# Kernel tuning notes

Measured on AMD Instinct MI355X. Metric: run time of the kernel, lower is better.

Reference implementation:

```python
import jax, jax.numpy as jnp
import numpy as np

SL, BS, E, H, PF, STRIDE, SHIFT = 2048, 2, 1024, 16, 16, 1, 0
DH = E // H  # 64


def setup_inputs() -> dict:
    key = jax.random.key(0)
    ks = jax.random.split(key, 6)
    s = 0.02
    return {
        'x': jax.random.normal(ks[0], (SL, BS, E), jnp.float32),
        'ln_g': jnp.ones((E,), jnp.float32),
        'ln_b': jnp.zeros((E,), jnp.float32),
        'Wq': jax.random.normal(ks[1], (E, E), jnp.float32) * s,
        'bq': jnp.zeros((E,), jnp.float32),
        'Wk': jax.random.normal(ks[2], (E, E), jnp.float32) * s,
        'bk': jnp.zeros((E,), jnp.float32),
        'Wv': jax.random.normal(ks[3], (E, E), jnp.float32) * s,
        'bv': jnp.zeros((E,), jnp.float32),
        'Wo': jax.random.normal(ks[4], (E, E), jnp.float32) * s,
        'bo': jnp.zeros((E,), jnp.float32),
    }


def _layernorm(x, g, b, eps=1e-5):
    m = x.mean(-1, keepdims=True)
    v = jnp.var(x, axis=-1, keepdims=True)
    return (x - m) * jax.lax.rsqrt(v + eps) * g + b


def _sparsify(context, h):
    # faithful to sparsify(): r = (arange(h)+1)*stride - pf + shift (+ arange(pf)), mod c
    c = context.shape[0]
    base = (jnp.arange(h) + 1) * STRIDE - PF + SHIFT          # [h]
    idx = (base[None, :] + jnp.arange(PF)[:, None]) % c       # [pf, h]
    return context[idx.reshape(-1)].reshape(PF, h, context.shape[1], context.shape[2])


def reference(x, ln_g, ln_b, Wq, bq, Wk, bk, Wv, bv, Wo, bo):
    sl, bs, e = x.shape
    residual = x
    xn = _layernorm(x, ln_g, ln_b)
    # gather pf-sized local context window per query position (modular wrap)
    fetch = _sparsify(xn, sl)                                  # [pf, sl, bs, E]
    # per-token query (length-1) attending to its pf gathered keys
    q = (xn @ Wq + bq).reshape(sl, bs, H, DH)                  # [sl,bs,H,dh]
    k = (fetch @ Wk + bk).reshape(PF, sl, bs, H, DH)           # [pf,sl,bs,H,dh]
    v = (fetch @ Wv + bv).reshape(PF, sl, bs, H, DH)
    scale = 1.0 / jnp.sqrt(jnp.float32(DH))
    scores = jnp.einsum('sbhd,psbhd->sbhp', q, k) * scale      # [sl,bs,H,pf]
    attn = jax.nn.softmax(scores, axis=-1)
    out = jnp.einsum('sbhp,psbhd->sbhd', attn, v).reshape(sl, bs, e)
    out = out @ Wo + bo                                        # output projection
    # dropout is a no-op in eval
    return residual + out
```

## Files before the change

### kernel.cpp

```cpp
#include <hip/hip_runtime.h>
#include <cstdint>
#include <cstddef>

#define SLEN 2048
#define BSZ  2
#define EDIM 1024
#define NHEAD 16
#define DHEAD 64
#define PFW  16
#define NTOK (SLEN*BSZ)

#define BM 128
#define BN 128
#define BK 32

typedef __attribute__((ext_vector_type(8))) short short8;
typedef __attribute__((ext_vector_type(4))) float floatx4;

__device__ __forceinline__ short f2bf(float f) {
  union { float f; uint32_t u; } v; v.f = f;
  uint32_t r = v.u + 0x7fffu + ((v.u >> 16) & 1u);
  return (short)(r >> 16);
}
__device__ __forceinline__ float bf2f(short s) {
  union { uint32_t u; float f; } v; v.u = ((uint32_t)(uint16_t)s) << 16;
  return v.f;
}

__device__ __forceinline__ void async16(const void* g, void* l) {
  __builtin_amdgcn_global_load_lds((const __attribute__((address_space(1))) void*)g,
                                   (__attribute__((address_space(3))) void*)l,
                                   16, 0, 0);
}

__global__ __launch_bounds__(256) void transpose_kernel(
    const float* __restrict__ W0, const float* __restrict__ W1,
    const float* __restrict__ W2, const float* __restrict__ W3,
    short* __restrict__ Wt_base)
{
  const int z = blockIdx.z;
  const float* W = (z == 0) ? W0 : (z == 1) ? W1 : (z == 2) ? W2 : W3;
  short* Wt = Wt_base + (size_t)z * EDIM * EDIM;

  __shared__ float tile[32][33];
  const int tx = threadIdx.x & 31;
  const int ty = threadIdx.x >> 5;
  const int n0 = blockIdx.x * 32;
  const int k0 = blockIdx.y * 32;

#pragma unroll
  for (int i = 0; i < 4; ++i)
    tile[ty + i * 8][tx] = W[(size_t)(k0 + ty + i * 8) * EDIM + n0 + tx];
  __syncthreads();
#pragma unroll
  for (int i = 0; i < 4; ++i)
    Wt[(size_t)(n0 + ty + i * 8) * EDIM + k0 + tx] = f2bf(tile[tx][ty + i * 8]);
}

__global__ __launch_bounds__(256) void layernorm_kernel(
    const float* __restrict__ x, const float* __restrict__ g,
    const float* __restrict__ b, short* __restrict__ xn)
{
  const int row = blockIdx.x;
  const int tid = threadIdx.x;
  const float4 v = ((const float4*)(x + (size_t)row * EDIM))[tid];

  float s  = v.x + v.y + v.z + v.w;
  float ss = v.x * v.x + v.y * v.y + v.z * v.z + v.w * v.w;
#pragma unroll
  for (int off = 32; off; off >>= 1) {
    s  += __shfl_xor(s, off);
    ss += __shfl_xor(ss, off);
  }
  __shared__ float ws_s[4], ws_ss[4];
  const int lane = tid & 63, wave = tid >> 6;
  if (lane == 0) { ws_s[wave] = s; ws_ss[wave] = ss; }
  __syncthreads();
  s  = ws_s[0] + ws_s[1] + ws_s[2] + ws_s[3];
  ss = ws_ss[0] + ws_ss[1] + ws_ss[2] + ws_ss[3];

  const float mean = s * (1.0f / EDIM);
  const float var  = ss * (1.0f / EDIM) - mean * mean;
  const float rs   = rsqrtf(var + 1e-5f);

  const float4 gv = ((const float4*)g)[tid];
  const float4 bv = ((const float4*)b)[tid];
  short4 o;
  o.x = f2bf((v.x - mean) * rs * gv.x + bv.x);
  o.y = f2bf((v.y - mean) * rs * gv.y + bv.y);
  o.z = f2bf((v.z - mean) * rs * gv.z + bv.z);
  o.w = f2bf((v.w - mean) * rs * gv.w + bv.w);
  ((short4*)(xn + (size_t)row * EDIM))[tid] = o;
}

__device__ __forceinline__ void gemm_mainloop(
    const short* __restrict__ A, const short* __restrict__ Bt, int K,
    int bm, int bn, short* As, short* Bs, floatx4 (&acc)[4][4])
{
  const int tid  = threadIdx.x;
  const int lane = tid & 63;
  const int wave = tid >> 6;

  const int lrow = lane >> 2;
  const int lcol = (lane & 3) * 8;
  const short* gA0 = A  + (size_t)(bm + wave * 32 + lrow) * K + lcol;
  const short* gA1 = gA0 + (size_t)16 * K;
  const short* gB0 = Bt + (size_t)(bn + wave * 32 + lrow) * K + lcol;
  const short* gB1 = gB0 + (size_t)16 * K;
  short* lA0 = As + wave * 1024;
  short* lA1 = lA0 + 512;
  short* lB0 = Bs + wave * 1024;
  short* lB1 = lB0 + 512;

  const int wm = (wave >> 1) * 64;
  const int wn = (wave & 1) * 64;
  const int fr = lane & 15;
  const int fq = (lane >> 4) * 8;

  for (int k0 = 0; k0 < K; k0 += BK) {
    async16(gA0, lA0); async16(gA1, lA1);
    async16(gB0, lB0); async16(gB1, lB1);
    gA0 += BK; gA1 += BK; gB0 += BK; gB1 += BK;
    __syncthreads();

    short8 af[4], bf[4];
#pragma unroll
    for (int mi = 0; mi < 4; ++mi)
      af[mi] = *(const short8*)(As + (size_t)(wm + mi * 16 + fr) * BK + fq);
#pragma unroll
    for (int ni = 0; ni < 4; ++ni)
      bf[ni] = *(const short8*)(Bs + (size_t)(wn + ni * 16 + fr) * BK + fq);
#pragma unroll
    for (int mi = 0; mi < 4; ++mi)
#pragma unroll
      for (int ni = 0; ni < 4; ++ni)
        acc[mi][ni] = __builtin_amdgcn_mfma_f32_16x16x32_bf16(
            af[mi], bf[ni], acc[mi][ni], 0, 0, 0);
    __syncthreads();
  }
}

__global__ __launch_bounds__(256) void gemm_qkv(
    const short* __restrict__ xn, const short* __restrict__ Wt_base,
    const float* __restrict__ bq, const float* __restrict__ bk,
    const float* __restrict__ bv, short* __restrict__ qkv_base)
{
  __shared__ short As[BM * BK];
  __shared__ short Bs[BN * BK];
  const int z = blockIdx.z;
  const short* Bt   = Wt_base + (size_t)z * EDIM * EDIM;
  const float* bias = (z == 0) ? bq : (z == 1) ? bk : bv;
  short* out        = qkv_base + (size_t)z * NTOK * EDIM;

  const int bm = blockIdx.x * BM;
  const int bn = blockIdx.y * BN;
  floatx4 acc[4][4];
#pragma unroll
  for (int i = 0; i < 4; ++i)
#pragma unroll
    for (int j = 0; j < 4; ++j) { floatx4 zz = {0.f, 0.f, 0.f, 0.f}; acc[i][j] = zz; }

  gemm_mainloop(xn, Bt, EDIM, bm, bn, As, Bs, acc);

  const int lane = threadIdx.x & 63;
  const int wave = threadIdx.x >> 6;
  const int wm = (wave >> 1) * 64, wn = (wave & 1) * 64;
  const int r0 = bm + wm + ((lane >> 4) * 4);
  const int c0 = bn + wn + (lane & 15);
#pragma unroll
  for (int mi = 0; mi < 4; ++mi)
#pragma unroll
    for (int ni = 0; ni < 4; ++ni) {
      const floatx4 v = acc[mi][ni];
      const int col = c0 + ni * 16;
      const float bb = bias[col];
#pragma unroll
      for (int r = 0; r < 4; ++r) {
        const int row = r0 + mi * 16 + r;
        out[(size_t)row * EDIM + col] = f2bf(v[r] + bb);
      }
    }
}

__global__ __launch_bounds__(256) void gemm_o(
    const short* __restrict__ Aattn, const short* __restrict__ Wot,
    const float* __restrict__ bo, const float* __restrict__ residual,
    float* __restrict__ out)
{
  __shared__ short As[BM * BK];
  __shared__ short Bs[BN * BK];
  const int bm = blockIdx.x * BM;
  const int bn = blockIdx.y * BN;
  floatx4 acc[4][4];
#pragma unroll
  for (int i = 0; i < 4; ++i)
#pragma unroll
    for (int j = 0; j < 4; ++j) { floatx4 zz = {0.f, 0.f, 0.f, 0.f}; acc[i][j] = zz; }

  gemm_mainloop(Aattn, Wot, EDIM, bm, bn, As, Bs, acc);

  const int lane = threadIdx.x & 63;
  const int wave = threadIdx.x >> 6;
  const int wm = (wave >> 1) * 64, wn = (wave & 1) * 64;
  const int r0 = bm + wm + ((lane >> 4) * 4);
  const int c0 = bn + wn + (lane & 15);
#pragma unroll
  for (int mi = 0; mi < 4; ++mi)
#pragma unroll
    for (int ni = 0; ni < 4; ++ni) {
      const floatx4 v = acc[mi][ni];
      const int col = c0 + ni * 16;
      const float bb = bo[col];
#pragma unroll
      for (int r = 0; r < 4; ++r) {
        const int row = r0 + mi * 16 + r;
        const size_t idx = (size_t)row * EDIM + col;
        out[idx] = residual[idx] + v[r] + bb;
      }
    }
}

#define VT_LD 80
#define PB_LD 40

__global__ __launch_bounds__(256) void attn_mfma(
    const short* __restrict__ Q, const short* __restrict__ K,
    const short* __restrict__ V, short* __restrict__ O)
{
  const int tid  = threadIdx.x;
  const int lane = tid & 63;
  const int wave = tid >> 6;
  const int quad = lane >> 4;
  const int l16  = lane & 15;

  const int bh = blockIdx.y;
  const int h  = bh & (NHEAD - 1);
  const int b  = bh >> 4;
  const int s_blk = blockIdx.x * 64;
  const int col0  = h * DHEAD;

  __shared__ __align__(16) short VT[64 * VT_LD];
  __shared__ __align__(16) short Pb[4][16 * PB_LD];

  for (int task = tid; task < 320; task += 256) {
    const int kp  = task >> 3;
    const int dg  = task & 7;
    const int kk0 = kp * 2;
    int sA = s_blk - 15 + kk0;
    int sB = sA + 1;
    if (sA < 0) sA += SLEN;  if (sA >= SLEN) sA -= SLEN;
    if (sB < 0) sB += SLEN;  if (sB >= SLEN) sB -= SLEN;
    const short8 vA = *(const short8*)(V + (size_t)(sA * BSZ + b) * EDIM + col0 + dg * 8);
    const short8 vB = *(const short8*)(V + (size_t)(sB * BSZ + b) * EDIM + col0 + dg * 8);
#pragma unroll
    for (int j = 0; j < 8; ++j) {
      const int d = dg * 8 + j;
      const uint32_t pack = (uint32_t)(uint16_t)vA[j] | ((uint32_t)(uint16_t)vB[j] << 16);
      *(uint32_t*)&VT[d * VT_LD + kk0] = pack;
    }
  }

  const int sw = s_blk + wave * 16;
  short8 aq[2];
  {
    const size_t base = (size_t)((sw + l16) * BSZ + b) * EDIM + col0 + quad * 8;
    aq[0] = *(const short8*)(Q + base);
    aq[1] = *(const short8*)(Q + base + 32);
  }
  short8 bkf[2][2];
#pragma unroll
  for (int T = 0; T < 2; ++T) {
    int ks = sw - 15 + T * 16 + l16;
    if (ks < 0) ks += SLEN;
    if (ks >= SLEN) ks -= SLEN;
    const size_t base = (size_t)(ks * BSZ + b) * EDIM + col0 + quad * 8;
    bkf[T][0] = *(const short8*)(K + base);
    bkf[T][1] = *(const short8*)(K + base + 32);
  }

  floatx4 S[2];
  { floatx4 zz = {0.f, 0.f, 0.f, 0.f}; S[0] = zz; S[1] = zz; }
#pragma unroll
  for (int T = 0; T < 2; ++T) {
    S[T] = __builtin_amdgcn_mfma_f32_16x16x32_bf16(aq[0], bkf[T][0], S[T], 0, 0, 0);
    S[T] = __builtin_amdgcn_mfma_f32_16x16x32_bf16(aq[1], bkf[T][1], S[T], 0, 0, 0);
  }

  float sc[2][4];
#pragma unroll
  for (int T = 0; T < 2; ++T)
#pragma unroll
    for (int r = 0; r < 4; ++r) {
      const int m = quad * 4 + r;
      const int c = T * 16 + l16;
      const int d = c - m;
      sc[T][r] = (d >= 0 && d <= 15) ? S[T][r] * 0.125f : -1e30f;
    }
  float mx[4], sm[4];
#pragma unroll
  for (int r = 0; r < 4; ++r) mx[r] = fmaxf(sc[0][r], sc[1][r]);
#pragma unroll
  for (int off = 1; off <= 8; off <<= 1)
#pragma unroll
    for (int r = 0; r < 4; ++r) mx[r] = fmaxf(mx[r], __shfl_xor(mx[r], off));
  float p[2][4];
#pragma unroll
  for (int r = 0; r < 4; ++r) {
    p[0][r] = __expf(sc[0][r] - mx[r]);
    p[1][r] = __expf(sc[1][r] - mx[r]);
    sm[r] = p[0][r] + p[1][r];
  }
#pragma unroll
  for (int off = 1; off <= 8; off <<= 1)
#pragma unroll
    for (int r = 0; r < 4; ++r) sm[r] += __shfl_xor(sm[r], off);

  __syncthreads();

  short* Pw = Pb[wave];
#pragma unroll
  for (int T = 0; T < 2; ++T)
#pragma unroll
    for (int r = 0; r < 4; ++r) {
      const int m = quad * 4 + r;
      const int c = T * 16 + l16;
      Pw[m * PB_LD + c] = f2bf(p[T][r]);
    }
  __syncthreads();
  const short8 ap = *(const short8*)(Pw + l16 * PB_LD + quad * 8);

  floatx4 Oacc[4];
  { floatx4 zz = {0.f, 0.f, 0.f, 0.f}; Oacc[0] = zz; Oacc[1] = zz; Oacc[2] = zz; Oacc[3] = zz; }
#pragma unroll
  for (int nt = 0; nt < 4; ++nt) {
    const short8 bv = *(const short8*)(VT + (nt * 16 + l16) * VT_LD + wave * 16 + quad * 8);
    Oacc[nt] = __builtin_amdgcn_mfma_f32_16x16x32_bf16(ap, bv, Oacc[nt], 0, 0, 0);
  }

#pragma unroll
  for (int nt = 0; nt < 4; ++nt)
#pragma unroll
    for (int r = 0; r < 4; ++r) {
      const int m = quad * 4 + r;
      const size_t idx = (size_t)((sw + m) * BSZ + b) * EDIM + col0 + nt * 16 + l16;
      O[idx] = f2bf(Oacc[nt][r] / sm[r]);
    }
}

extern "C" void kernel_launch(void* const* d_in, const int* in_sizes, int n_in,
                              void* d_out, int out_size, void* d_ws, size_t ws_size,
                              hipStream_t stream) {
  const float* x    = (const float*)d_in[0];
  const float* ln_g = (const float*)d_in[1];
  const float* ln_b = (const float*)d_in[2];
  const float* Wq   = (const float*)d_in[3];
  const float* bq   = (const float*)d_in[4];
  const float* Wk   = (const float*)d_in[5];
  const float* bk   = (const float*)d_in[6];
  const float* Wv   = (const float*)d_in[7];
  const float* bv   = (const float*)d_in[8];
  const float* Wo   = (const float*)d_in[9];
  const float* bo   = (const float*)d_in[10];
  float* out = (float*)d_out;

  char* ws = (char*)d_ws;
  short* xn   = (short*)(ws);
  short* Wt   = (short*)(ws + ((size_t)8  << 20));
  short* QKV  = (short*)(ws + ((size_t)16 << 20));
  short* attn = (short*)(ws + ((size_t)40 << 20));

  transpose_kernel<<<dim3(32, 32, 4), 256, 0, stream>>>(Wq, Wk, Wv, Wo, Wt);
  layernorm_kernel<<<NTOK, 256, 0, stream>>>(x, ln_g, ln_b, xn);
  gemm_qkv<<<dim3(NTOK / BM, EDIM / BN, 3), 256, 0, stream>>>(xn, Wt, bq, bk, bv, QKV);
  attn_mfma<<<dim3(SLEN / 64, BSZ * NHEAD), 256, 0, stream>>>(
      QKV, QKV + (size_t)NTOK * EDIM, QKV + (size_t)2 * NTOK * EDIM, attn);
  gemm_o<<<dim3(NTOK / BM, EDIM / BN), 256, 0, stream>>>(
      attn, Wt + (size_t)3 * EDIM * EDIM, bo, x, out);
}
```

Measured before the change: 162.1 us.

## Merge layernorm and weight transpose into one launch; shrink output GEMM tile to 64 rows

The layernorm and the four weight-transpose launches are merged into one prep kernel whose block index picks which job each block does, removing one kernel launch and letting both jobs share the GPU. The output projection GEMM tile drops from 128x128 to 64x128, doubling its grid from 256 to 512 blocks so more of the CUs are busy. The shared mainloop helper is inlined into each GEMM. The smaller tile lowers data reuse per block and adds more global loads in exchange for the extra parallelism.

```diff
diff --git a/kernel.cpp b/kernel.cpp
--- a/kernel.cpp
+++ b/kernel.cpp
@@ -10,8 +10,6 @@
 #define PFW  16
 #define NTOK (SLEN*BSZ)
 
-#define BM 128
-#define BN 128
 #define BK 32
 
 typedef __attribute__((ext_vector_type(8))) short short8;
@@ -33,110 +31,64 @@
                                    16, 0, 0);
 }
 
-__global__ __launch_bounds__(256) void transpose_kernel(
+__global__ __launch_bounds__(256) void prep_kernel(
+    const float* __restrict__ x, const float* __restrict__ g,
+    const float* __restrict__ b, short* __restrict__ xn,
     const float* __restrict__ W0, const float* __restrict__ W1,
     const float* __restrict__ W2, const float* __restrict__ W3,
     short* __restrict__ Wt_base)
 {
-  const int z = blockIdx.z;
-  const float* W = (z == 0) ? W0 : (z == 1) ? W1 : (z == 2) ? W2 : W3;
-  short* Wt = Wt_base + (size_t)z * EDIM * EDIM;
-
-  __shared__ float tile[32][33];
-  const int tx = threadIdx.x & 31;
-  const int ty = threadIdx.x >> 5;
-  const int n0 = blockIdx.x * 32;
-  const int k0 = blockIdx.y * 32;
-
-#pragma unroll
-  for (int i = 0; i < 4; ++i)
-    tile[ty + i * 8][tx] = W[(size_t)(k0 + ty + i * 8) * EDIM + n0 + tx];
-  __syncthreads();
-#pragma unroll
-  for (int i = 0; i < 4; ++i)
-    Wt[(size_t)(n0 + ty + i * 8) * EDIM + k0 + tx] = f2bf(tile[tx][ty + i * 8]);
-}
-
-__global__ __launch_bounds__(256) void layernorm_kernel(
-    const float* __restrict__ x, const float* __restrict__ g,
-    const float* __restrict__ b, short* __restrict__ xn)
-{
-  const int row = blockIdx.x;
+  const int bid = blockIdx.x;
   const int tid = threadIdx.x;
-  const float4 v = ((const float4*)(x + (size_t)row * EDIM))[tid];
-
-  float s  = v.x + v.y + v.z + v.w;
-  float ss = v.x * v.x + v.y * v.y + v.z * v.z + v.w * v.w;
-#pragma unroll
-  for (int off = 32; off; off >>= 1) {
-    s  += __shfl_xor(s, off);
-    ss += __shfl_xor(ss, off);
-  }
-  __shared__ float ws_s[4], ws_ss[4];
-  const int lane = tid & 63, wave = tid >> 6;
-  if (lane == 0) { ws_s[wave] = s; ws_ss[wave] = ss; }
-  __syncthreads();
-  s  = ws_s[0] + ws_s[1] + ws_s[2] + ws_s[3];
-  ss = ws_ss[0] + ws_ss[1] + ws_ss[2] + ws_ss[3];
-
-  const float mean = s * (1.0f / EDIM);
-  const float var  = ss * (1.0f / EDIM) - mean * mean;
-  const float rs   = rsqrtf(var + 1e-5f);
-
-  const float4 gv = ((const float4*)g)[tid];
-  const float4 bv = ((const float4*)b)[tid];
-  short4 o;
-  o.x = f2bf((v.x - mean) * rs * gv.x + bv.x);
-  o.y = f2bf((v.y - mean) * rs * gv.y + bv.y);
-  o.z = f2bf((v.z - mean) * rs * gv.z + bv.z);
-  o.w = f2bf((v.w - mean) * rs * gv.w + bv.w);
-  ((short4*)(xn + (size_t)row * EDIM))[tid] = o;
-}
-
-__device__ __forceinline__ void gemm_mainloop(
-    const short* __restrict__ A, const short* __restrict__ Bt, int K,
-    int bm, int bn, short* As, short* Bs, floatx4 (&acc)[4][4])
-{
-  const int tid  = threadIdx.x;
-  const int lane = tid & 63;
-  const int wave = tid >> 6;
-
-  const int lrow = lane >> 2;
-  const int lcol = (lane & 3) * 8;
-  const short* gA0 = A  + (size_t)(bm + wave * 32 + lrow) * K + lcol;
-  const short* gA1 = gA0 + (size_t)16 * K;
-  const short* gB0 = Bt + (size_t)(bn + wave * 32 + lrow) * K + lcol;
-  const short* gB1 = gB0 + (size_t)16 * K;
-  short* lA0 = As + wave * 1024;
-  short* lA1 = lA0 + 512;
-  short* lB0 = Bs + wave * 1024;
-  short* lB1 = lB0 + 512;
-
-  const int wm = (wave >> 1) * 64;
-  const int wn = (wave & 1) * 64;
-  const int fr = lane & 15;
-  const int fq = (lane >> 4) * 8;
-
-  for (int k0 = 0; k0 < K; k0 += BK) {
-    async16(gA0, lA0); async16(gA1, lA1);
-    async16(gB0, lB0); async16(gB1, lB1);
-    gA0 += BK; gA1 += BK; gB0 += BK; gB1 += BK;
-    __syncthreads();
-
-    short8 af[4], bf[4];
-#pragma unroll
-    for (int mi = 0; mi < 4; ++mi)
-      af[mi] = *(const short8*)(As + (size_t)(wm + mi * 16 + fr) * BK + fq);
-#pragma unroll
-    for (int ni = 0; ni < 4; ++ni)
-      bf[ni] = *(const short8*)(Bs + (size_t)(wn + ni * 16 + fr) * BK + fq);
-#pragma unroll
-    for (int mi = 0; mi < 4; ++mi)
-#pragma unroll
-      for (int ni = 0; ni < 4; ++ni)
-        acc[mi][ni] = __builtin_amdgcn_mfma_f32_16x16x32_bf16(
-            af[mi], bf[ni], acc[mi][ni], 0, 0, 0);
-    __syncthreads();
+
+  if (bid < NTOK) {
+    const int row = bid;
+    const float4 v = ((const float4*)(x + (size_t)row * EDIM))[tid];
+    float s  = v.x + v.y + v.z + v.w;
+    float ss = v.x * v.x + v.y * v.y + v.z * v.z + v.w * v.w;
+#pragma unroll
+    for (int off = 32; off; off >>= 1) {
+      s  += __shfl_xor(s, off);
+      ss += __shfl_xor(ss, off);
+    }
+    __shared__ float ws_s[4], ws_ss[4];
+    const int lane = tid & 63, wave = tid >> 6;
+    if (lane == 0) { ws_s[wave] = s; ws_ss[wave] = ss; }
+    __syncthreads();
+    s  = ws_s[0] + ws_s[1] + ws_s[2] + ws_s[3];
+    ss = ws_ss[0] + ws_ss[1] + ws_ss[2] + ws_ss[3];
+
+    const float mean = s * (1.0f / EDIM);
+    const float var  = ss * (1.0f / EDIM) - mean * mean;
+    const float rs   = rsqrtf(var + 1e-5f);
+
+    const float4 gv = ((const float4*)g)[tid];
+    const float4 bv = ((const float4*)b)[tid];
+    short4 o;
+    o.x = f2bf((v.x - mean) * rs * gv.x + bv.x);
+    o.y = f2bf((v.y - mean) * rs * gv.y + bv.y);
+    o.z = f2bf((v.z - mean) * rs * gv.z + bv.z);
+    o.w = f2bf((v.w - mean) * rs * gv.w + bv.w);
+    ((short4*)(xn + (size_t)row * EDIM))[tid] = o;
+  } else {
+    const int t = bid - NTOK;
+    const int z = t >> 10;
+    const int rem = t & 1023;
+    const int n0 = (rem & 31) * 32;
+    const int k0 = (rem >> 5) * 32;
+    const float* W = (z == 0) ? W0 : (z == 1) ? W1 : (z == 2) ? W2 : W3;
+    short* Wt = Wt_base + (size_t)z * EDIM * EDIM;
+
+    __shared__ float tile[32][33];
+    const int tx = tid & 31;
+    const int ty = tid >> 5;
+#pragma unroll
+    for (int i = 0; i < 4; ++i)
+      tile[ty + i * 8][tx] = W[(size_t)(k0 + ty + i * 8) * EDIM + n0 + tx];
+    __syncthreads();
+#pragma unroll
+    for (int i = 0; i < 4; ++i)
+      Wt[(size_t)(n0 + ty + i * 8) * EDIM + k0 + tx] = f2bf(tile[tx][ty + i * 8]);
   }
 }
 
@@ -145,26 +97,63 @@
     const float* __restrict__ bq, const float* __restrict__ bk,
     const float* __restrict__ bv, short* __restrict__ qkv_base)
 {
-  __shared__ short As[BM * BK];
-  __shared__ short Bs[BN * BK];
+  __shared__ short As[128 * BK];
+  __shared__ short Bs[128 * BK];
   const int z = blockIdx.z;
   const short* Bt   = Wt_base + (size_t)z * EDIM * EDIM;
   const float* bias = (z == 0) ? bq : (z == 1) ? bk : bv;
   short* out        = qkv_base + (size_t)z * NTOK * EDIM;
 
-  const int bm = blockIdx.x * BM;
-  const int bn = blockIdx.y * BN;
+  const int bm = blockIdx.x * 128;
+  const int bn = blockIdx.y * 128;
+  const int tid  = threadIdx.x;
+  const int lane = tid & 63;
+  const int wave = tid >> 6;
+
   floatx4 acc[4][4];
 #pragma unroll
   for (int i = 0; i < 4; ++i)
 #pragma unroll
     for (int j = 0; j < 4; ++j) { floatx4 zz = {0.f, 0.f, 0.f, 0.f}; acc[i][j] = zz; }
 
-  gemm_mainloop(xn, Bt, EDIM, bm, bn, As, Bs, acc);
-
-  const int lane = threadIdx.x & 63;
-  const int wave = threadIdx.x >> 6;
-  const int wm = (wave >> 1) * 64, wn = (wave & 1) * 64;
+  const int lrow = lane >> 2;
+  const int lcol = (lane & 3) * 8;
+  const short* gA0 = xn + (size_t)(bm + wave * 32 + lrow) * EDIM + lcol;
+  const short* gA1 = gA0 + (size_t)16 * EDIM;
+  const short* gB0 = Bt + (size_t)(bn + wave * 32 + lrow) * EDIM + lcol;
+  const short* gB1 = gB0 + (size_t)16 * EDIM;
+  short* lA0 = As + wave * 1024;
+  short* lA1 = lA0 + 512;
+  short* lB0 = Bs + wave * 1024;
+  short* lB1 = lB0 + 512;
+
+  const int wm = (wave >> 1) * 64;
+  const int wn = (wave & 1) * 64;
+  const int fr = lane & 15;
+  const int fq = (lane >> 4) * 8;
+
+  for (int k0 = 0; k0 < EDIM; k0 += BK) {
+    async16(gA0, lA0); async16(gA1, lA1);
+    async16(gB0, lB0); async16(gB1, lB1);
+    gA0 += BK; gA1 += BK; gB0 += BK; gB1 += BK;
+    __syncthreads();
+
+    short8 af[4], bf[4];
+#pragma unroll
+    for (int mi = 0; mi < 4; ++mi)
+      af[mi] = *(const short8*)(As + (size_t)(wm + mi * 16 + fr) * BK + fq);
+#pragma unroll
+    for (int ni = 0; ni < 4; ++ni)
+      bf[ni] = *(const short8*)(Bs + (size_t)(wn + ni * 16 + fr) * BK + fq);
+#pragma unroll
+    for (int mi = 0; mi < 4; ++mi)
+#pragma unroll
+      for (int ni = 0; ni < 4; ++ni)
+        acc[mi][ni] = __builtin_amdgcn_mfma_f32_16x16x32_bf16(
+            af[mi], bf[ni], acc[mi][ni], 0, 0, 0);
+    __syncthreads();
+  }
+
   const int r0 = bm + wm + ((lane >> 4) * 4);
   const int c0 = bn + wn + (lane & 15);
 #pragma unroll
@@ -187,25 +176,60 @@
     const float* __restrict__ bo, const float* __restrict__ residual,
     float* __restrict__ out)
 {
-  __shared__ short As[BM * BK];
-  __shared__ short Bs[BN * BK];
-  const int bm = blockIdx.x * BM;
-  const int bn = blockIdx.y * BN;
-  floatx4 acc[4][4];
-#pragma unroll
-  for (int i = 0; i < 4; ++i)
+  __shared__ short As[64 * BK];
+  __shared__ short Bs[128 * BK];
+  const int bm = blockIdx.x * 64;
+  const int bn = blockIdx.y * 128;
+  const int tid  = threadIdx.x;
+  const int lane = tid & 63;
+  const int wave = tid >> 6;
+
+  floatx4 acc[2][4];
+#pragma unroll
+  for (int i = 0; i < 2; ++i)
 #pragma unroll
     for (int j = 0; j < 4; ++j) { floatx4 zz = {0.f, 0.f, 0.f, 0.f}; acc[i][j] = zz; }
 
-  gemm_mainloop(Aattn, Wot, EDIM, bm, bn, As, Bs, acc);
-
-  const int lane = threadIdx.x & 63;
-  const int wave = threadIdx.x >> 6;
-  const int wm = (wave >> 1) * 64, wn = (wave & 1) * 64;
+  const int lrow = lane >> 2;
+  const int lcol = (lane & 3) * 8;
+  const short* gA0 = Aattn + (size_t)(bm + wave * 16 + lrow) * EDIM + lcol;
+  const short* gB0 = Wot + (size_t)(bn + wave * 32 + lrow) * EDIM + lcol;
+  const short* gB1 = gB0 + (size_t)16 * EDIM;
+  short* lA0 = As + wave * 512;
+  short* lB0 = Bs + wave * 1024;
+  short* lB1 = lB0 + 512;
+
+  const int wm = (wave >> 1) * 32;
+  const int wn = (wave & 1) * 64;
+  const int fr = lane & 15;
+  const int fq = (lane >> 4) * 8;
+
+  for (int k0 = 0; k0 < EDIM; k0 += BK) {
+    async16(gA0, lA0);
+    async16(gB0, lB0); async16(gB1, lB1);
+    gA0 += BK; gB0 += BK; gB1 += BK;
+    __syncthreads();
+
+    short8 af[2], bf[4];
+#pragma unroll
+    for (int mi = 0; mi < 2; ++mi)
+      af[mi] = *(const short8*)(As + (size_t)(wm + mi * 16 + fr) * BK + fq);
+#pragma unroll
+    for (int ni = 0; ni < 4; ++ni)
+      bf[ni] = *(const short8*)(Bs + (size_t)(wn + ni * 16 + fr) * BK + fq);
+#pragma unroll
+    for (int mi = 0; mi < 2; ++mi)
+#pragma unroll
+      for (int ni = 0; ni < 4; ++ni)
+        acc[mi][ni] = __builtin_amdgcn_mfma_f32_16x16x32_bf16(
+            af[mi], bf[ni], acc[mi][ni], 0, 0, 0);
+    __syncthreads();
+  }
+
   const int r0 = bm + wm + ((lane >> 4) * 4);
   const int c0 = bn + wn + (lane & 15);
 #pragma unroll
-  for (int mi = 0; mi < 4; ++mi)
+  for (int mi = 0; mi < 2; ++mi)
 #pragma unroll
     for (int ni = 0; ni < 4; ++ni) {
       const floatx4 v = acc[mi][ni];
@@ -369,11 +393,10 @@
   short* QKV  = (short*)(ws + ((size_t)16 << 20));
   short* attn = (short*)(ws + ((size_t)40 << 20));
 
-  transpose_kernel<<<dim3(32, 32, 4), 256, 0, stream>>>(Wq, Wk, Wv, Wo, Wt);
-  layernorm_kernel<<<NTOK, 256, 0, stream>>>(x, ln_g, ln_b, xn);
-  gemm_qkv<<<dim3(NTOK / BM, EDIM / BN, 3), 256, 0, stream>>>(xn, Wt, bq, bk, bv, QKV);
+  prep_kernel<<<NTOK + 4096, 256, 0, stream>>>(x, ln_g, ln_b, xn, Wq, Wk, Wv, Wo, Wt);
+  gemm_qkv<<<dim3(NTOK / 128, EDIM / 128, 3), 256, 0, stream>>>(xn, Wt, bq, bk, bv, QKV);
   attn_mfma<<<dim3(SLEN / 64, BSZ * NHEAD), 256, 0, stream>>>(
       QKV, QKV + (size_t)NTOK * EDIM, QKV + (size_t)2 * NTOK * EDIM, attn);
-  gemm_o<<<dim3(NTOK / BM, EDIM / BN), 256, 0, stream>>>(
+  gemm_o<<<dim3(NTOK / 64, EDIM / 128), 256, 0, stream>>>(
       attn, Wt + (size_t)3 * EDIM * EDIM, bo, x, out);
 }
```

After: 159.6 us. No clear change (-1.5%).
